# Optimization experiments

Hardware: AMD Instinct MI355X
Metric: run time of the kernel (lower is better)

Reference implementation:

```python
import jax, jax.numpy as jnp
import numpy as np

B = 8192
N_IN = 1024
N_OUT = 1024
IN_OUT = N_IN + N_OUT


def setup_inputs() -> dict:
    key = jax.random.key(0)
    ks = jax.random.split(key, 11)
    s = 1.0 / np.sqrt(IN_OUT)  # nn.Linear default init scale
    inp = {
        "x": jax.random.normal(ks[0], (B, N_IN), dtype=jnp.float32),
        "out_tm1": jax.random.normal(ks[1], (B, N_OUT), dtype=jnp.float32),
        "state_tm1": jax.random.normal(ks[2], (B, N_OUT), dtype=jnp.float32),
        "Wf": jax.random.uniform(ks[3], (IN_OUT, N_OUT), jnp.float32, -s, s),
        "bf": jax.random.uniform(ks[4], (N_OUT,), jnp.float32, -s, s),
        "Wi": jax.random.uniform(ks[5], (IN_OUT, N_OUT), jnp.float32, -s, s),
        "bi": jax.random.uniform(ks[6], (N_OUT,), jnp.float32, -s, s),
        "Wc": jax.random.uniform(ks[7], (IN_OUT, N_OUT), jnp.float32, -s, s),
        "bc": jax.random.uniform(ks[8], (N_OUT,), jnp.float32, -s, s),
        "Wo": jax.random.uniform(ks[9], (IN_OUT, N_OUT), jnp.float32, -s, s),
        "bo": jax.random.uniform(ks[10], (N_OUT,), jnp.float32, -s, s),
    }
    return inp


def reference(x, out_tm1, state_tm1, Wf, bf, Wi, bi, Wc, bc, Wo, bo):
    xh = jnp.concatenate((x, out_tm1), axis=-1)  # [B, n_in+n_out]
    f = jax.nn.sigmoid(xh @ Wf + bf)             # forget gate
    i = jax.nn.sigmoid(xh @ Wi + bi)             # input gate
    c = jnp.tanh(xh @ Wc + bc)                   # candidates
    o = jax.nn.sigmoid(xh @ Wo + bo)             # output gate
    new_state = state_tm1 * f + i * c
    output_t = o * jnp.tanh(new_state)
    return (output_t, new_state)
```

## Files before the change

kernel.cpp:

```cpp
#include <hip/hip_runtime.h>

#define B_DIM 8192
#define NOUT  1024
#define KDIM  2048

typedef __bf16 bf16x8 __attribute__((ext_vector_type(8)));
typedef float  f32x4  __attribute__((ext_vector_type(4)));

__device__ __forceinline__ unsigned short f2bf(float f) {
  unsigned int u = __float_as_uint(f);
  u += 0x7fff + ((u >> 16) & 1);
  return (unsigned short)(u >> 16);
}
__device__ __forceinline__ float sigmoid_f(float x) {
  return 1.0f / (1.0f + __expf(-x));
}
__device__ __forceinline__ float tanh_f(float x) {
  return 1.0f - 2.0f / (__expf(2.0f * x) + 1.0f);
}
__device__ __forceinline__ void gload_lds16(const void* g, void* l) {
  __builtin_amdgcn_global_load_lds(
      (const __attribute__((address_space(1))) void*)g,
      (__attribute__((address_space(3))) void*)l, 16, 0, 0);
}

__device__ __forceinline__ int cimap(int g, int n) {
  return ((n >> 4) << 6) | ((g & 3) << 4) | (n & 15);
}

__global__ void pack_xh_kernel(const float* __restrict__ x,
                               const float* __restrict__ h,
                               unsigned short* __restrict__ xh) {
  const long total = (long)B_DIM * KDIM / 4;
  for (long i = (long)blockIdx.x * blockDim.x + threadIdx.x; i < total;
       i += (long)gridDim.x * blockDim.x) {
    long e = i * 4;
    int b = (int)(e >> 11);
    int c = (int)(e & 2047);
    float4 v = (c < 1024)
        ? *reinterpret_cast<const float4*>(x + (long)b * 1024 + c)
        : *reinterpret_cast<const float4*>(h + (long)b * 1024 + (c - 1024));
    ushort4 o;
    o.x = f2bf(v.x); o.y = f2bf(v.y); o.z = f2bf(v.z); o.w = f2bf(v.w);
    *reinterpret_cast<ushort4*>(xh + e) = o;
  }
}

__global__ void transpose_w_kernel(const float* __restrict__ Wf,
                                   const float* __restrict__ Wi,
                                   const float* __restrict__ Wc,
                                   const float* __restrict__ Wo,
                                   unsigned short* __restrict__ wt) {
  __shared__ float tile[32][33];
  const int g = blockIdx.z;
  const float* W = (g == 0) ? Wf : (g == 1) ? Wi : (g == 2) ? Wc : Wo;
  const int n0 = blockIdx.x * 32;
  const int k0 = blockIdx.y * 32;
  const int tx = threadIdx.x, ty = threadIdx.y;
#pragma unroll
  for (int r = ty; r < 32; r += 8)
    tile[r][tx] = W[(long)(k0 + r) * NOUT + n0 + tx];
  __syncthreads();
#pragma unroll
  for (int r = ty; r < 32; r += 8) {
    int ci = cimap(g, n0 + r);
    wt[(long)ci * KDIM + k0 + tx] = f2bf(tile[tx][r]);
  }
}

__device__ __forceinline__ void stage6(const char* xh_b, const char* wt_b,
                                       long aoff, long boff, int kt,
                                       char* lds, int sbase, int tid) {
  const long kb = (long)kt * 64;
#pragma unroll
  for (int r = 0; r < 2; ++r)
    gload_lds16(xh_b + aoff + (long)r * 64 * 4096 + kb,
                lds + sbase + r * 4096 + tid * 16);
#pragma unroll
  for (int r = 0; r < 4; ++r)
    gload_lds16(wt_b + boff + (long)r * 64 * 4096 + kb,
                lds + sbase + 8192 + r * 4096 + tid * 16);
}

#define LOAD_FRAGS(S)                                                       \
  _Pragma("unroll") for (int mi = 0; mi < 8; ++mi)                          \
    af[mi] = *reinterpret_cast<const bf16x8*>(                              \
        lds + (S)*24576 + mi * 1024 + rdoff);                               \
  _Pragma("unroll") for (int ni = 0; ni < 4; ++ni)                          \
    bq[ni] = *reinterpret_cast<const bf16x8*>(                              \
        lds + (S)*24576 + 8192 + wn * 4096 + ni * 1024 + rdoff);

#define MFMA32()                                                            \
  _Pragma("unroll") for (int mi = 0; mi < 8; ++mi)                          \
  _Pragma("unroll") for (int ni = 0; ni < 4; ++ni)                          \
    acc[mi][ni] = __builtin_amdgcn_mfma_f32_16x16x32_bf16(                  \
        af[mi], bq[ni], acc[mi][ni], 0, 0, 0);

#define ITER(RS, WS, KST)                                                   \
  LOAD_FRAGS(RS)                                                            \
  stage6(xh_b, wt_b, aoff, boff, (KST), lds, (WS)*24576, tid);              \
  asm volatile("s_waitcnt vmcnt(6) lgkmcnt(0)" ::: "memory");               \
  __builtin_amdgcn_sched_barrier(0);                                        \
  __builtin_amdgcn_s_barrier();                                             \
  __builtin_amdgcn_sched_barrier(0);                                        \
  __builtin_amdgcn_s_setprio(1);                                            \
  MFMA32()                                                                  \
  __builtin_amdgcn_s_setprio(0);                                            \
  __builtin_amdgcn_sched_barrier(0);

__global__ __launch_bounds__(256, 2)
void lstm_gemm_kernel(const unsigned short* __restrict__ xh,
                      const unsigned short* __restrict__ wt,
                      const float* __restrict__ state,
                      const float* __restrict__ bfp,
                      const float* __restrict__ bip,
                      const float* __restrict__ bcp,
                      const float* __restrict__ bop,
                      float* __restrict__ out) {
  __shared__ __attribute__((aligned(128))) char lds[73728];

  const int tid  = threadIdx.x;
  const int lane = tid & 63;
  const int wn   = tid >> 6;

  const int wgid = blockIdx.y * 16 + blockIdx.x;
  const int j    = wgid >> 3;
  const int xcd  = wgid & 7;
  const int bx   = (xcd << 1) | (j & 1);
  const int by   = j >> 1;
  const long m0  = (long)by * 128;
  const long c0  = (long)bx * 256;

  const int  rsub = tid >> 2;
  const int  gsw  = ((tid & 3) ^ (rsub & 3)) << 4;
  const long aoff = (m0 + rsub) * 4096 + gsw;
  const long boff = (c0 + rsub) * 4096 + gsw;

  const int rdoff = (lane & 15) * 64 + (((lane >> 4) ^ (lane & 3)) << 4);

  const char* xh_b = (const char*)xh;
  const char* wt_b = (const char*)wt;

  f32x4  acc[8][4] = {};
  bf16x8 af[8];
  bf16x8 bq[4];

  stage6(xh_b, wt_b, aoff, boff, 0, lds, 0,     tid);
  stage6(xh_b, wt_b, aoff, boff, 1, lds, 24576, tid);
  asm volatile("s_waitcnt vmcnt(6)" ::: "memory");
  __builtin_amdgcn_sched_barrier(0);
  __builtin_amdgcn_s_barrier();
  __builtin_amdgcn_sched_barrier(0);

  for (int t = 0; t < 63; t += 3) {
    const int k2 = t + 2;
    const int k3 = (t + 3 > 63) ? 63 : t + 3;
    const int k4 = (t + 4 > 63) ? 63 : t + 4;
    ITER(0, 2, k2)
    ITER(1, 0, k3)
    ITER(2, 1, k4)
  }
  LOAD_FRAGS(0)
  asm volatile("s_waitcnt lgkmcnt(0)" ::: "memory");
  __builtin_amdgcn_sched_barrier(0);
  __builtin_amdgcn_s_setprio(1);
  MFMA32()
  __builtin_amdgcn_s_setprio(0);
  asm volatile("s_waitcnt vmcnt(0)" ::: "memory");

  const int   nout = (bx * 4 + wn) * 16 + (lane & 15);
  const int   rsub4 = (lane >> 4) << 2;
  const float bfv = bfp[nout], biv = bip[nout];
  const float bcv = bcp[nout], bov = bop[nout];
  float* out2 = out + (long)B_DIM * NOUT;
#pragma unroll
  for (int mi = 0; mi < 8; ++mi)
#pragma unroll
    for (int v = 0; v < 4; ++v) {
      const long row = m0 + mi * 16 + rsub4 + v;
      float fg = sigmoid_f(acc[mi][0][v] + bfv);
      float ig = sigmoid_f(acc[mi][1][v] + biv);
      float cg = tanh_f   (acc[mi][2][v] + bcv);
      float og = sigmoid_f(acc[mi][3][v] + bov);
      float st = state[row * NOUT + nout];
      float ns = st * fg + ig * cg;
      out [row * NOUT + nout] = og * tanh_f(ns);
      out2[row * NOUT + nout] = ns;
    }
}

extern "C" void kernel_launch(void* const* d_in, const int* in_sizes, int n_in,
                              void* d_out, int out_size, void* d_ws, size_t ws_size,
                              hipStream_t stream) {
  const float* x     = (const float*)d_in[0];
  const float* h     = (const float*)d_in[1];
  const float* state = (const float*)d_in[2];
  const float* Wf    = (const float*)d_in[3];
  const float* bfp   = (const float*)d_in[4];
  const float* Wi    = (const float*)d_in[5];
  const float* bip   = (const float*)d_in[6];
  const float* Wc    = (const float*)d_in[7];
  const float* bcp   = (const float*)d_in[8];
  const float* Wo    = (const float*)d_in[9];
  const float* bop   = (const float*)d_in[10];
  float* out = (float*)d_out;

  unsigned short* xh = (unsigned short*)d_ws;
  unsigned short* wt = (unsigned short*)((char*)d_ws + (size_t)B_DIM * KDIM * 2);

  hipLaunchKernelGGL(pack_xh_kernel, dim3(2048), dim3(256), 0, stream, x, h, xh);
  hipLaunchKernelGGL(transpose_w_kernel, dim3(NOUT / 32, KDIM / 32, 4),
                     dim3(32, 8), 0, stream, Wf, Wi, Wc, Wo, wt);
  hipLaunchKernelGGL(lstm_gemm_kernel, dim3(16, 64), dim3(256), 0, stream,
                     xh, wt, state, bfp, bip, bcp, bop, out);
}
```

Baseline: 173.0 us.

## Reorder GEMM pipeline stages, new LDS swizzle and workgroup-to-tile mapping

Each iteration now issues the global-to-LDS prefetch before the fragment reads and moves the vmcnt wait and workgroup barrier after the MFMA block. This lets the compiler overlap LDS fragment reads with MFMAs instead of waiting for all of them first. It also changes the LDS staging layout and XOR swizzle (two rows per 8-thread group, new read offsets) to cut bank conflicts. The workgroup-to-tile mapping becomes an XCD-major swizzle, which changes L2 locality. The risk is that the new swizzle or barrier placement reduces reuse or adds stalls.

```diff
diff --git a/kernel.cpp b/kernel.cpp
--- a/kernel.cpp
+++ b/kernel.cpp
@@ -3,6 +3,7 @@
 #define B_DIM 8192
 #define NOUT  1024
 #define KDIM  2048
+#define SLOT  24576
 
 typedef __bf16 bf16x8 __attribute__((ext_vector_type(8)));
 typedef float  f32x4  __attribute__((ext_vector_type(4)));
@@ -68,27 +69,26 @@
   }
 }
 
-__device__ __forceinline__ void stage6(const char* xh_b, const char* wt_b,
-                                       long aoff, long boff, int kt,
-                                       char* lds, int sbase, int tid) {
-  const long kb = (long)kt * 64;
-#pragma unroll
-  for (int r = 0; r < 2; ++r)
-    gload_lds16(xh_b + aoff + (long)r * 64 * 4096 + kb,
-                lds + sbase + r * 4096 + tid * 16);
-#pragma unroll
-  for (int r = 0; r < 4; ++r)
-    gload_lds16(wt_b + boff + (long)r * 64 * 4096 + kb,
-                lds + sbase + 8192 + r * 4096 + tid * 16);
-}
+#define SB() __builtin_amdgcn_sched_barrier(0);
 
 #define LOAD_FRAGS(S)                                                       \
   _Pragma("unroll") for (int mi = 0; mi < 8; ++mi)                          \
     af[mi] = *reinterpret_cast<const bf16x8*>(                              \
-        lds + (S)*24576 + mi * 1024 + rdoff);                               \
+        lds + (S)*SLOT + mi * 1024 + laneRC);                               \
   _Pragma("unroll") for (int ni = 0; ni < 4; ++ni)                          \
     bq[ni] = *reinterpret_cast<const bf16x8*>(                              \
-        lds + (S)*24576 + 8192 + wn * 4096 + ni * 1024 + rdoff);
+        lds + (S)*SLOT + 8192 + wn * 4096 + ni * 1024 + laneRC);
+
+#define STAGE6(WS, KT) {                                                    \
+  const long kb_ = (long)(KT) * 64 + scol;                                  \
+  const char* ab_ = xh_b + (m0 + srow0) * 4096 + kb_;                       \
+  const char* bb_ = wt_b + (c0 + srow0) * 4096 + kb_;                       \
+  gload_lds16(ab_,             lds + (WS)*SLOT +         t16);              \
+  gload_lds16(ab_ +  64L*4096, lds + (WS)*SLOT + 4096  + t16);              \
+  gload_lds16(bb_,             lds + (WS)*SLOT + 8192  + t16);              \
+  gload_lds16(bb_ +  64L*4096, lds + (WS)*SLOT + 12288 + t16);              \
+  gload_lds16(bb_ + 128L*4096, lds + (WS)*SLOT + 16384 + t16);              \
+  gload_lds16(bb_ + 192L*4096, lds + (WS)*SLOT + 20480 + t16); }
 
 #define MFMA32()                                                            \
   _Pragma("unroll") for (int mi = 0; mi < 8; ++mi)                          \
@@ -96,17 +96,16 @@
     acc[mi][ni] = __builtin_amdgcn_mfma_f32_16x16x32_bf16(                  \
         af[mi], bq[ni], acc[mi][ni], 0, 0, 0);
 
-#define ITER(RS, WS, KST)                                                   \
+#define ITER(RS, WS, KT)                                                    \
+  STAGE6(WS, KT)                                                            \
   LOAD_FRAGS(RS)                                                            \
-  stage6(xh_b, wt_b, aoff, boff, (KST), lds, (WS)*24576, tid);              \
-  asm volatile("s_waitcnt vmcnt(6) lgkmcnt(0)" ::: "memory");               \
-  __builtin_amdgcn_sched_barrier(0);                                        \
-  __builtin_amdgcn_s_barrier();                                             \
-  __builtin_amdgcn_sched_barrier(0);                                        \
   __builtin_amdgcn_s_setprio(1);                                            \
   MFMA32()                                                                  \
   __builtin_amdgcn_s_setprio(0);                                            \
-  __builtin_amdgcn_sched_barrier(0);
+  asm volatile("s_waitcnt vmcnt(6)" ::: "memory");                          \
+  SB()                                                                      \
+  __builtin_amdgcn_s_barrier();                                             \
+  SB()
 
 __global__ __launch_bounds__(256, 2)
 void lstm_gemm_kernel(const unsigned short* __restrict__ xh,
@@ -124,19 +123,20 @@
   const int wn   = tid >> 6;
 
   const int wgid = blockIdx.y * 16 + blockIdx.x;
-  const int j    = wgid >> 3;
-  const int xcd  = wgid & 7;
-  const int bx   = (xcd << 1) | (j & 1);
-  const int by   = j >> 1;
+  const int swz  = (wgid & 7) * 128 + (wgid >> 3);
+  const int by   = swz >> 4;
+  const int bx   = swz & 15;
   const long m0  = (long)by * 128;
   const long c0  = (long)bx * 256;
 
-  const int  rsub = tid >> 2;
-  const int  gsw  = ((tid & 3) ^ (rsub & 3)) << 4;
-  const long aoff = (m0 + rsub) * 4096 + gsw;
-  const long boff = (c0 + rsub) * 4096 + gsw;
-
-  const int rdoff = (lane & 15) * 64 + (((lane >> 4) ^ (lane & 3)) << 4);
+  const int key    = (lane >> 1) & 7;
+  const int slotsw = (((lane & 1) << 2) | (lane >> 4)) ^ key;
+  const int laneRC = key * 128 + slotsw * 16;
+
+  const int vsw   = (tid & 7) ^ ((tid >> 3) & 7);
+  const int srow0 = ((tid >> 3) << 1) + (vsw >> 2);
+  const int scol  = (vsw & 3) << 4;
+  const int t16   = tid * 16;
 
   const char* xh_b = (const char*)xh;
   const char* wt_b = (const char*)wt;
@@ -145,28 +145,26 @@
   bf16x8 af[8];
   bf16x8 bq[4];
 
-  stage6(xh_b, wt_b, aoff, boff, 0, lds, 0,     tid);
-  stage6(xh_b, wt_b, aoff, boff, 1, lds, 24576, tid);
+  STAGE6(0, 0)
+  STAGE6(1, 1)
   asm volatile("s_waitcnt vmcnt(6)" ::: "memory");
-  __builtin_amdgcn_sched_barrier(0);
+  SB()
   __builtin_amdgcn_s_barrier();
-  __builtin_amdgcn_sched_barrier(0);
+  SB()
 
   for (int t = 0; t < 63; t += 3) {
-    const int k2 = t + 2;
     const int k3 = (t + 3 > 63) ? 63 : t + 3;
     const int k4 = (t + 4 > 63) ? 63 : t + 4;
-    ITER(0, 2, k2)
+    ITER(0, 2, t + 2)
     ITER(1, 0, k3)
     ITER(2, 1, k4)
   }
   LOAD_FRAGS(0)
-  asm volatile("s_waitcnt lgkmcnt(0)" ::: "memory");
-  __builtin_amdgcn_sched_barrier(0);
   __builtin_amdgcn_s_setprio(1);
   MFMA32()
   __builtin_amdgcn_s_setprio(0);
-  asm volatile("s_waitcnt vmcnt(0)" ::: "memory");
+  asm volatile("s_waitcnt vmcnt(0) lgkmcnt(0)" ::: "memory");
+  SB()
 
   const int   nout = (bx * 4 + wn) * 16 + (lane & 15);
   const int   rsub4 = (lane >> 4) << 2;
```

After: 175.4 us. No clear change (+1.4%).
